# Kernel optimization log

Measured on AMD Instinct MI355X. Metric: run time of the kernel, lower is better.

## Reference

```python
import jax, jax.numpy as jnp
import numpy as np

N = 100000
E = 1600000
D_IN = 128
D_HID = 32
NEG_SLOPE = 0.2


def _glorot(key, shape):
    fan_in, fan_out = shape[0], shape[-1]
    lim = jnp.sqrt(6.0 / (fan_in + fan_out))
    return jax.random.uniform(key, shape, jnp.float32, -lim, lim)


def setup_inputs() -> dict:
    key = jax.random.key(0)
    ks = jax.random.split(key, 10)
    x = jax.random.normal(ks[0], (N, D_IN), jnp.float32)
    edge_index = jax.random.randint(ks[1], (2, E), 0, N, jnp.int64)
    return {
        "x": x,
        "edge_index": edge_index,
        "W1_l": _glorot(ks[2], (D_IN, D_HID)),
        "W1_r": _glorot(ks[3], (D_IN, D_HID)),
        "att1": _glorot(ks[4], (D_HID,)),
        "b1": jnp.zeros((D_HID,), jnp.float32),
        "W2_l": _glorot(ks[5], (D_HID, D_HID)),
        "W2_r": _glorot(ks[6], (D_HID, D_HID)),
        "att2": _glorot(ks[7], (D_HID,)),
        "b2": jnp.zeros((D_HID,), jnp.float32),
    }


def _segment_softmax(logits, seg, num_segments):
    m = jax.ops.segment_max(logits, seg, num_segments=num_segments)
    m = jnp.where(jnp.isfinite(m), m, 0.0)
    ex = jnp.exp(logits - m[seg])
    s = jax.ops.segment_sum(ex, seg, num_segments=num_segments)
    return ex / (s[seg] + 1e-16)


def _gatv2(x, edge_index, W_l, W_r, att, b):
    # GATv2Conv, heads=1, add_self_loops=False, share_weights=False
    src, dst = edge_index[0], edge_index[1]
    x_l = x @ W_l  # source transform [N, D_HID]
    x_r = x @ W_r  # target transform [N, D_HID]
    # per-edge attention logit: att . leaky_relu(x_l[j] + x_r[i])
    h = x_l[src] + x_r[dst]  # [E, D_HID]
    e = jnp.where(h > 0, h, NEG_SLOPE * h) @ att  # [E]
    alpha = _segment_softmax(e, dst, x.shape[0])  # softmax over incoming edges
    out = jax.ops.segment_sum(alpha[:, None] * x_l[src], dst,
                              num_segments=x.shape[0])
    return out + b


def reference(x, edge_index, W1_l, W1_r, att1, b1, W2_l, W2_r, att2, b2):
    h = _gatv2(x, edge_index, W1_l, W1_r, att1, b1)
    h = jax.nn.relu(h)
    return _gatv2(h, edge_index, W2_l, W2_r, att2, b2)
```

## Files before the change

### kernel.cpp

```cpp
#include <hip/hip_runtime.h>
#include <hip/hip_bf16.h>

#define D_HID 32
#define D_IN 128
#define NEG 0.2f
#define BSH 7
#define BSZ 128
#define MAXB 1024
#define MAXD 128

typedef unsigned short u16;
typedef __attribute__((ext_vector_type(8))) short short8;
typedef __attribute__((ext_vector_type(4))) float float4v;

__device__ __forceinline__ float b2f(u16 u){
  union { unsigned int i; float f; } c; c.i = ((unsigned int)u) << 16; return c.f;
}

__device__ __forceinline__ u16 f2b_rne(float f){
  union { float f; unsigned int u; } c; c.f = f;
  unsigned int u = c.u;
  return (u16)((u + 0x7FFFu + ((u >> 16) & 1u)) >> 16);
}

__device__ __forceinline__ void split_bf16(float v, u16& hi, u16& lo){
  hi = f2b_rne(v);
  lo = f2b_rne(v - b2f(hi));
}

__device__ __forceinline__ float ldf(const void* __restrict__ p, int f32, long long i){
  return f32 ? ((const float*)p)[i] : b2f(((const u16*)p)[i]);
}

__device__ __forceinline__ int atomAddI(int* p, int v){
  return __hip_atomic_fetch_add(p, v, __ATOMIC_RELAXED, __HIP_MEMORY_SCOPE_AGENT);
}

__device__ __forceinline__ float red8(float p){
  p += __int_as_float(__builtin_amdgcn_update_dpp(
         0, __float_as_int(p), 0xB1, 0xF, 0xF, true));
  p += __int_as_float(__builtin_amdgcn_update_dpp(
         0, __float_as_int(p), 0x4E, 0xF, 0xF, true));
  p += __int_as_float(__builtin_amdgcn_ds_swizzle(
         __float_as_int(p), 0x101F));
  return p;
}

__device__ __forceinline__ float edge_ev(const float4 xv, const float4 xrk,
                                         const float4 attk){
  float hx = xv.x + xrk.x; hx = fmaxf(hx, NEG*hx);
  float hy = xv.y + xrk.y; hy = fmaxf(hy, NEG*hy);
  float hz = xv.z + xrk.z; hz = fmaxf(hz, NEG*hz);
  float hw = xv.w + xrk.w; hw = fmaxf(hw, NEG*hw);
  float p = hx*attk.x;
  p = fmaf(hy, attk.y, p);
  p = fmaf(hz, attk.z, p);
  p = fmaf(hw, attk.w, p);
  p = red8(p);
  p = fminf(p, 60.f);
  return __expf(p);
}

__global__ void detect_flags(const int* __restrict__ ei, const u16* __restrict__ xw,
                             int* __restrict__ flags){
  __shared__ int insane_s, nz_s;
  int t = threadIdx.x;
  if (t == 0){ insane_s = 0; nz_s = 0; }
  __syncthreads();
  int pred = (t < 64) ? (ei[2*t+1] != 0) : 0;
  int e = (xw[t] >> 7) & 0xFF;
  int bad = (e < 100 || e > 140) ? 1 : 0;
  #pragma unroll
  for (int off = 32; off >= 1; off >>= 1){
    bad  += __shfl_down(bad,  off, 64);
    pred += __shfl_down(pred, off, 64);
  }
  if ((t & 63) == 0){
    atomicAdd(&insane_s, bad);
    atomicAdd(&nz_s, pred);
  }
  __syncthreads();
  if (t == 0){
    flags[0] = (nz_s == 0) ? 1 : 0;
    flags[1] = (insane_s > 16) ? 1 : 0;
  }
}

__device__ __forceinline__ void edge_nodes(const int* __restrict__ ei, int E_, int is64,
                                           int e, int& src, int& dst){
  if (is64){ src = ei[2*e]; dst = ei[2*E_ + 2*e]; }
  else     { src = ei[e];   dst = ei[E_ + e]; }
}

__global__ void prep_wfrag(const void* __restrict__ Wl, const void* __restrict__ Wr,
                           const int* __restrict__ flags, int K,
                           uint4* __restrict__ whi, uint4* __restrict__ wlo){
  int t = blockIdx.x * blockDim.x + threadIdx.x;
  int KS = K >> 5;
  int total = 4 * KS * 64;
  if (t >= total) return;
  int lane = t & 63;
  int rem = t >> 6;
  int kstep = rem % KS;
  int ctile = rem / KS;
  int f32 = flags[1];
  int col = ctile * 16 + (lane & 15);
  int quad = lane >> 4;
  union { u16 s[8]; uint4 q; } ch, cl;
  #pragma unroll
  for (int j = 0; j < 8; ++j){
    int k = kstep*32 + quad*8 + j;
    float v = (col < 32) ? ldf(Wl, f32, (long long)k*D_HID + col)
                         : ldf(Wr, f32, (long long)k*D_HID + (col - 32));
    u16 hi, lo; split_bf16(v, hi, lo);
    ch.s[j] = hi; cl.s[j] = lo;
  }
  whi[rem*64 + lane] = ch.q;
  wlo[rem*64 + lane] = cl.q;
}

template<int K>
__global__ void mfma_gemm(const void* __restrict__ X,
                          const uint4* __restrict__ whi, const uint4* __restrict__ wlo,
                          const int* __restrict__ flags, int force_f32,
                          float* __restrict__ xl, float* __restrict__ xr, int N_)
{
  constexpr int KS = K >> 5;
  int tile = blockIdx.x * (blockDim.x >> 6) + (threadIdx.x >> 6);
  if (tile * 16 >= N_) return;
  int lane = threadIdx.x & 63;
  int quad = lane >> 4;
  int m = tile*16 + (lane & 15);
  if (m >= N_) m = N_ - 1;
  int f32 = force_f32 | flags[1];

  float4v acc[4];
  #pragma unroll
  for (int c = 0; c < 4; ++c) acc[c] = (float4v){0.f,0.f,0.f,0.f};

  #pragma unroll
  for (int ks = 0; ks < KS; ++ks){
    long long base = (long long)m * K + ks*32 + quad*8;
    float av[8];
    if (f32){
      const float4* xp = (const float4*)((const float*)X + base);
      float4 t0 = xp[0], t1 = xp[1];
      av[0]=t0.x; av[1]=t0.y; av[2]=t0.z; av[3]=t0.w;
      av[4]=t1.x; av[5]=t1.y; av[6]=t1.z; av[7]=t1.w;
    } else {
      union { uint4 q; u16 s[8]; } c8;
      c8.q = *(const uint4*)((const u16*)X + base);
      #pragma unroll
      for (int j = 0; j < 8; ++j) av[j] = b2f(c8.s[j]);
    }
    short8 ahi, alo;
    #pragma unroll
    for (int j = 0; j < 8; ++j){
      u16 hi, lo; split_bf16(av[j], hi, lo);
      ahi[j] = (short)hi; alo[j] = (short)lo;
    }
    #pragma unroll
    for (int c = 0; c < 4; ++c){
      uint4 wh = whi[(c*KS + ks)*64 + lane];
      uint4 wl = wlo[(c*KS + ks)*64 + lane];
      short8 bh = *(short8*)&wh;
      short8 bl = *(short8*)&wl;
      acc[c] = __builtin_amdgcn_mfma_f32_16x16x32_bf16(ahi, bh, acc[c], 0, 0, 0);
      acc[c] = __builtin_amdgcn_mfma_f32_16x16x32_bf16(ahi, bl, acc[c], 0, 0, 0);
      acc[c] = __builtin_amdgcn_mfma_f32_16x16x32_bf16(alo, bh, acc[c], 0, 0, 0);
    }
  }

  #pragma unroll
  for (int c = 0; c < 4; ++c){
    int col = c*16 + (lane & 15);
    float* dst = (col < 32) ? xl : xr;
    int kk = col & 31;
    #pragma unroll
    for (int r = 0; r < 4; ++r){
      int node = tile*16 + quad*4 + r;
      if (node < N_) dst[(size_t)node*D_HID + kk] = acc[c][r];
    }
  }
}

__global__ void bucket_count(const int* __restrict__ ei, const int* __restrict__ flags,
                             int* __restrict__ gcnt, int E_, int B_){
  __shared__ int hist[MAXB];
  for (int i = threadIdx.x; i < B_; i += 256) hist[i] = 0;
  __syncthreads();
  int chunk = (E_ + gridDim.x - 1) / gridDim.x;
  int s = blockIdx.x * chunk;
  int e = s + chunk; if (e > E_) e = E_;
  int is64 = flags[0];
  for (int i = s + (int)threadIdx.x; i < e; i += 256){
    int dst = is64 ? ei[2*E_ + 2*i] : ei[E_ + i];
    atomicAdd(&hist[dst >> BSH], 1);
  }
  __syncthreads();
  for (int i = threadIdx.x; i < B_; i += 256)
    if (hist[i]) (void)atomAddI(&gcnt[i], hist[i]);
}

__global__ void scan_buckets(const int* __restrict__ gcnt, int* __restrict__ offsets,
                             int* __restrict__ cursor, int B_){
  __shared__ int sd[1024];
  int t = threadIdx.x;
  int v = (t < B_) ? gcnt[t] : 0;
  sd[t] = v;
  __syncthreads();
  for (int off = 1; off < 1024; off <<= 1){
    int tmp = (t >= off) ? sd[t-off] : 0;
    __syncthreads();
    sd[t] += tmp;
    __syncthreads();
  }
  if (t < B_){
    int excl = sd[t] - v;
    offsets[t] = excl;
    cursor[t]  = excl;
    if (t == B_-1) offsets[B_] = sd[t];
  }
}

__global__ void bucket_scatter(const int* __restrict__ ei, const int* __restrict__ flags,
                               int* __restrict__ cursor, unsigned* __restrict__ seg,
                               int E_, int B_){
  __shared__ int hist[MAXB];
  __shared__ int bbase[MAXB];
  for (int i = threadIdx.x; i < B_; i += 256) hist[i] = 0;
  __syncthreads();
  int chunk = (E_ + gridDim.x - 1) / gridDim.x;
  int s = blockIdx.x * chunk;
  int e = s + chunk; if (e > E_) e = E_;
  int is64 = flags[0];
  for (int i = s + (int)threadIdx.x; i < e; i += 256){
    int dst = is64 ? ei[2*E_ + 2*i] : ei[E_ + i];
    atomicAdd(&hist[dst >> BSH], 1);
  }
  __syncthreads();
  for (int i = threadIdx.x; i < B_; i += 256){
    int c = hist[i];
    bbase[i] = c ? atomAddI(&cursor[i], c) : 0;
  }
  __syncthreads();
  for (int i = threadIdx.x; i < B_; i += 256) hist[i] = 0;
  __syncthreads();
  for (int i = s + (int)threadIdx.x; i < e; i += 256){
    int src, dst;
    edge_nodes(ei, E_, is64, i, src, dst);
    int b = dst >> BSH;
    int pos = bbase[b] + atomicAdd(&hist[b], 1);
    seg[pos] = ((unsigned)src << BSH) | (unsigned)(dst & (BSZ-1));
  }
}

__global__ void bucket_finalize(const unsigned* __restrict__ seg,
                                const int* __restrict__ offsets,
                                int* __restrict__ row, int* __restrict__ csr_src,
                                int* __restrict__ dhist,
                                int N_, int B_){
  __shared__ int hist[BSZ];
  __shared__ int sc[BSZ];
  __shared__ int loff[BSZ];
  __shared__ int dh[MAXD];
  int b = blockIdx.x;
  int t = threadIdx.x;
  int base = offsets[b], cnt = offsets[b+1] - base;
  if (t < BSZ) hist[t] = 0;
  if (t < MAXD) dh[t] = 0;
  __syncthreads();
  for (int i = t; i < cnt; i += 256)
    atomicAdd(&hist[seg[base+i] & (BSZ-1)], 1);
  __syncthreads();
  if (t < BSZ){
    sc[t] = hist[t];
    int node = b*BSZ + t;
    if (node < N_) atomicAdd(&dh[min(hist[t], MAXD-1)], 1);
  }
  __syncthreads();
  for (int off = 1; off < BSZ; off <<= 1){
    int tmp = (t < BSZ && t >= off) ? sc[t-off] : 0;
    __syncthreads();
    if (t < BSZ) sc[t] += tmp;
    __syncthreads();
  }
  if (t < BSZ){
    int excl = sc[t] - hist[t];
    loff[t] = excl;
    int node = b*BSZ + t;
    if (node <= N_) row[node] = base + excl;
  }
  if (b == B_-1 && t == 0) row[N_] = offsets[B_];
  __syncthreads();
  for (int i = t; i < cnt; i += 256){
    unsigned en = seg[base+i];
    int dl = en & (BSZ-1);
    int pos = atomicAdd(&loff[dl], 1);
    csr_src[base + pos] = (int)en;
  }
  __syncthreads();
  if (t < MAXD && dh[t]) (void)atomAddI(&dhist[t], dh[t]);
}

__global__ void scan_deg(const int* __restrict__ dhist, int* __restrict__ dcur){
  __shared__ int sd[MAXD];
  int t = threadIdx.x;
  int v = dhist[t];
  sd[t] = v;
  __syncthreads();
  for (int off = 1; off < MAXD; off <<= 1){
    int tmp = (t >= off) ? sd[t-off] : 0;
    __syncthreads();
    sd[t] += tmp;
    __syncthreads();
  }
  dcur[t] = sd[t] - v;
}

__global__ void deg_scatter(const int* __restrict__ row, int* __restrict__ dcur,
                            int* __restrict__ perm, int N_){
  __shared__ int h[MAXD];
  __shared__ int base[MAXD];
  int t = threadIdx.x;
  int chunk = (N_ + gridDim.x - 1) / gridDim.x;
  int s = blockIdx.x * chunk;
  int e = s + chunk; if (e > N_) e = N_;
  if (t < MAXD) h[t] = 0;
  __syncthreads();
  for (int n = s + t; n < e; n += 256){
    int d = min(row[n+1] - row[n], MAXD-1);
    atomicAdd(&h[d], 1);
  }
  __syncthreads();
  if (t < MAXD){
    int c = h[t];
    base[t] = c ? atomAddI(&dcur[t], c) : 0;
  }
  __syncthreads();
  if (t < MAXD) h[t] = 0;
  __syncthreads();
  for (int n = s + t; n < e; n += 256){
    int d = min(row[n+1] - row[n], MAXD-1);
    int pos = base[d] + atomicAdd(&h[d], 1);
    perm[pos] = n;
  }
}

__global__ void gat_gather(const int* __restrict__ row, const unsigned* __restrict__ csrp,
                           const int* __restrict__ perm,
                           const float* __restrict__ xl, const float* __restrict__ xr,
                           const void* __restrict__ att, const void* __restrict__ bias,
                           const int* __restrict__ flags,
                           float* __restrict__ outp, int N_, int do_relu)
{
  int G = (blockIdx.x * blockDim.x + threadIdx.x) >> 3;
  if (G >= N_) return;
  int fl = threadIdx.x & 7;
  int f32 = flags[1];
  float4 attk;
  attk.x = ldf(att, f32, fl*4+0);
  attk.y = ldf(att, f32, fl*4+1);
  attk.z = ldf(att, f32, fl*4+2);
  attk.w = ldf(att, f32, fl*4+3);
  int n = perm[G];
  float4 xrk = *(const float4*)(xr + (size_t)n*D_HID + fl*4);
  int rs = row[n], re = row[n+1];
  const char* xlb = (const char*)xl;
  unsigned fo = (unsigned)(fl << 4);

  float4 acc = make_float4(0.f, 0.f, 0.f, 0.f);
  float ssum = 0.f;

  if (rs < re){
    int last = re - 1;
    unsigned c0 = csrp[rs];
    unsigned c1 = csrp[min(rs+1, last)];
    unsigned c2 = csrp[min(rs+2, last)];
    unsigned c3 = csrp[min(rs+3, last)];
    unsigned ca = csrp[min(rs+4, last)];
    unsigned cb = csrp[min(rs+5, last)];
    float4 xv0 = *(const float4*)(xlb + (c0 & ~127u) + fo);
    float4 xv1 = *(const float4*)(xlb + (c1 & ~127u) + fo);
    float4 xv2 = *(const float4*)(xlb + (c2 & ~127u) + fo);
    float4 xv3 = *(const float4*)(xlb + (c3 & ~127u) + fo);
    for (int i = rs; i < re; i += 2){
      float4 nx0 = *(const float4*)(xlb + (ca & ~127u) + fo);
      float4 nx1 = *(const float4*)(xlb + (cb & ~127u) + fo);
      unsigned na = csrp[min(i+6, last)];
      unsigned nb = csrp[min(i+7, last)];
      float ev0 = edge_ev(xv0, xrk, attk);
      ssum += ev0;
      acc.x = fmaf(ev0, xv0.x, acc.x);
      acc.y = fmaf(ev0, xv0.y, acc.y);
      acc.z = fmaf(ev0, xv0.z, acc.z);
      acc.w = fmaf(ev0, xv0.w, acc.w);
      float ev1 = edge_ev(xv1, xrk, attk);
      ev1 = (i + 1 <= last) ? ev1 : 0.f;
      ssum += ev1;
      acc.x = fmaf(ev1, xv1.x, acc.x);
      acc.y = fmaf(ev1, xv1.y, acc.y);
      acc.z = fmaf(ev1, xv1.z, acc.z);
      acc.w = fmaf(ev1, xv1.w, acc.w);
      xv0 = xv2; xv1 = xv3; xv2 = nx0; xv3 = nx1;
      ca = na; cb = nb;
    }
  }

  float inv = 1.0f / (ssum + 1e-16f);
  float4 o;
  o.x = acc.x*inv + ldf(bias, f32, fl*4+0);
  o.y = acc.y*inv + ldf(bias, f32, fl*4+1);
  o.z = acc.z*inv + ldf(bias, f32, fl*4+2);
  o.w = acc.w*inv + ldf(bias, f32, fl*4+3);
  if (do_relu){
    o.x = fmaxf(o.x, 0.f); o.y = fmaxf(o.y, 0.f);
    o.z = fmaxf(o.z, 0.f); o.w = fmaxf(o.w, 0.f);
  }
  *(float4*)(outp + (size_t)n*D_HID + fl*4) = o;
}

extern "C" void kernel_launch(void* const* d_in, const int* in_sizes, int n_in,
                              void* d_out, int out_size, void* d_ws, size_t ws_size,
                              hipStream_t stream)
{
  const void* x   = d_in[0];
  const int*  ei  = (const int*)d_in[1];
  const void* W1l = d_in[2];
  const void* W1r = d_in[3];
  const void* att1= d_in[4];
  const void* b1  = d_in[5];
  const void* W2l = d_in[6];
  const void* W2r = d_in[7];
  const void* att2= d_in[8];
  const void* b2  = d_in[9];
  float* out = (float*)d_out;

  int N_ = in_sizes[0] / D_IN;
  int E_ = in_sizes[1] / 2;
  int B_ = (N_ + BSZ - 1) / BSZ;

  char* ws = (char*)d_ws;
  size_t off = 0;
  auto carve = [&](size_t bytes) -> char* {
    char* p = ws + off;
    off += (bytes + 255) & ~(size_t)255;
    return p;
  };
  float*    xl      = (float*)   carve((size_t)N_ * D_HID * 4);
  float*    xr      = (float*)   carve((size_t)N_ * D_HID * 4);
  float*    h       = (float*)   carve((size_t)N_ * D_HID * 4);
  unsigned* seg     = (unsigned*)carve((size_t)E_ * 4);
  int*      csr_src = (int*)     carve((size_t)E_ * 4);
  int*      row     = (int*)     carve((size_t)(N_ + 1) * 4);
  int*      perm    = (int*)     carve((size_t)N_ * 4);
  int*      offsets = (int*)     carve((size_t)(MAXB + 1) * 4);
  int*      gcnt    = (int*)     carve((size_t)MAXB * 4);
  int*      cursor  = (int*)     carve((size_t)MAXB * 4);
  int*      dhist   = (int*)     carve((size_t)MAXD * 4);
  int*      dcur    = (int*)     carve((size_t)MAXD * 4);
  int*      flags   = (int*)     carve(256);
  uint4*    whi1    = (uint4*)   carve((size_t)4 * 4 * 64 * 16);
  uint4*    wlo1    = (uint4*)   carve((size_t)4 * 4 * 64 * 16);
  uint4*    whi2    = (uint4*)   carve((size_t)4 * 1 * 64 * 16);
  uint4*    wlo2    = (uint4*)   carve((size_t)4 * 1 * 64 * 16);

  const int tpb = 256;
  int gG = (N_ + 31) / 32;
  int tiles = (N_ + 15) / 16;
  int gT = (tiles + 3) / 4;

  detect_flags<<<1, 256, 0, stream>>>(ei, (const u16*)x, flags);

  prep_wfrag<<<4, 256, 0, stream>>>(W1l, W1r, flags, D_IN, whi1, wlo1);
  prep_wfrag<<<1, 256, 0, stream>>>(W2l, W2r, flags, D_HID, whi2, wlo2);

  hipMemsetAsync(gcnt, 0, (size_t)MAXB * 4, stream);
  hipMemsetAsync(dhist, 0, (size_t)MAXD * 4, stream);
  bucket_count<<<256, tpb, 0, stream>>>(ei, flags, gcnt, E_, B_);
  scan_buckets<<<1, 1024, 0, stream>>>(gcnt, offsets, cursor, B_);
  bucket_scatter<<<256, tpb, 0, stream>>>(ei, flags, cursor, seg, E_, B_);
  bucket_finalize<<<B_, tpb, 0, stream>>>(seg, offsets, row, csr_src, dhist, N_, B_);

  scan_deg<<<1, MAXD, 0, stream>>>(dhist, dcur);
  deg_scatter<<<64, tpb, 0, stream>>>(row, dcur, perm, N_);

  mfma_gemm<D_IN><<<gT, tpb, 0, stream>>>(x, whi1, wlo1, flags, 0, xl, xr, N_);
  gat_gather<<<gG, tpb, 0, stream>>>(row, (const unsigned*)csr_src, perm, xl, xr,
                                     att1, b1, flags, h, N_, 1);

  mfma_gemm<D_HID><<<gT, tpb, 0, stream>>>(h, whi2, wlo2, flags, 1, xl, xr, N_);
  gat_gather<<<gG, tpb, 0, stream>>>(row, (const unsigned*)csr_src, perm, xl, xr,
                                     att2, b2, flags, out, N_, 0);
}
```

Baseline: 275.9 us.

## Fuse CSR build stages into fewer launches and drop degree-sorted permutation

Merges flag detection with bucket counting, fuses the bucket scan, scatter and weight-fragment prep into one launch with each block redoing the scan redundantly, and co-schedules bucket finalization with the first-layer GEMM in one grid. It drops the degree histogram and node permutation, so the gather walks nodes in natural order, and it deepens the gather's edge prefetch from four to six rows. The intent is to cut launch count and serialization on a short pipeline, at the cost of redundant per-block scans and losing degree-balanced warp scheduling in the gather.

```diff
diff --git a/kernel.cpp b/kernel.cpp
--- a/kernel.cpp
+++ b/kernel.cpp
@@ -7,7 +7,7 @@
 #define BSH 7
 #define BSZ 128
 #define MAXB 1024
-#define MAXD 128
+#define SCATB 256
 
 typedef unsigned short u16;
 typedef __attribute__((ext_vector_type(8))) short short8;
@@ -61,41 +61,43 @@
   return __expf(p);
 }
 
-__global__ void detect_flags(const int* __restrict__ ei, const u16* __restrict__ xw,
-                             int* __restrict__ flags){
-  __shared__ int insane_s, nz_s;
+__global__ void __launch_bounds__(256)
+count_flags(const int* __restrict__ ei, const u16* __restrict__ xw,
+            int* __restrict__ gcnt, int* __restrict__ flags, int E_, int B_){
+  __shared__ int hist[MAXB];
+  __shared__ int nz_s, insane_s;
   int t = threadIdx.x;
-  if (t == 0){ insane_s = 0; nz_s = 0; }
-  __syncthreads();
-  int pred = (t < 64) ? (ei[2*t+1] != 0) : 0;
-  int e = (xw[t] >> 7) & 0xFF;
-  int bad = (e < 100 || e > 140) ? 1 : 0;
-  #pragma unroll
-  for (int off = 32; off >= 1; off >>= 1){
-    bad  += __shfl_down(bad,  off, 64);
-    pred += __shfl_down(pred, off, 64);
-  }
-  if ((t & 63) == 0){
-    atomicAdd(&insane_s, bad);
-    atomicAdd(&nz_s, pred);
-  }
-  __syncthreads();
-  if (t == 0){
-    flags[0] = (nz_s == 0) ? 1 : 0;
+  if (t == 0){ nz_s = 0; insane_s = 0; }
+  for (int i = t; i < B_; i += 256) hist[i] = 0;
+  __syncthreads();
+  if (t < 64 && ei[2*t+1] != 0) atomicAdd(&nz_s, 1);
+  if (blockIdx.x == 0){
+    int e = (xw[t] >> 7) & 0xFF;
+    if (e < 100 || e > 140) atomicAdd(&insane_s, 1);
+  }
+  __syncthreads();
+  int is64 = (nz_s == 0);
+  if (blockIdx.x == 0 && t == 0){
+    flags[0] = is64;
     flags[1] = (insane_s > 16) ? 1 : 0;
   }
-}
-
-__device__ __forceinline__ void edge_nodes(const int* __restrict__ ei, int E_, int is64,
-                                           int e, int& src, int& dst){
-  if (is64){ src = ei[2*e]; dst = ei[2*E_ + 2*e]; }
-  else     { src = ei[e];   dst = ei[E_ + e]; }
-}
-
-__global__ void prep_wfrag(const void* __restrict__ Wl, const void* __restrict__ Wr,
-                           const int* __restrict__ flags, int K,
-                           uint4* __restrict__ whi, uint4* __restrict__ wlo){
-  int t = blockIdx.x * blockDim.x + threadIdx.x;
+  int chunk = (E_ + gridDim.x - 1) / gridDim.x;
+  int s = blockIdx.x * chunk;
+  int e = s + chunk; if (e > E_) e = E_;
+  for (int i = s + t; i < e; i += 256){
+    int dst = is64 ? ei[2*E_ + 2*i] : ei[E_ + i];
+    atomicAdd(&hist[dst >> BSH], 1);
+  }
+  __syncthreads();
+  for (int i = t; i < B_; i += 256)
+    if (hist[i]) (void)atomAddI(&gcnt[i], hist[i]);
+}
+
+__device__ __forceinline__ void prep_body(const void* __restrict__ Wl,
+                                          const void* __restrict__ Wr,
+                                          int f32, int K,
+                                          uint4* __restrict__ whi,
+                                          uint4* __restrict__ wlo, int t){
   int KS = K >> 5;
   int total = 4 * KS * 64;
   if (t >= total) return;
@@ -103,7 +105,6 @@
   int rem = t >> 6;
   int kstep = rem % KS;
   int ctile = rem / KS;
-  int f32 = flags[1];
   int col = ctile * 16 + (lane & 15);
   int quad = lane >> 4;
   union { u16 s[8]; uint4 q; } ch, cl;
@@ -119,16 +120,123 @@
   wlo[rem*64 + lane] = cl.q;
 }
 
+__global__ void __launch_bounds__(256)
+scan_scatter_prep(const int* __restrict__ ei, const int* __restrict__ flags,
+                  const int* __restrict__ gcnt, int* __restrict__ cur0,
+                  unsigned* __restrict__ seg, int* __restrict__ offsets,
+                  const void* __restrict__ W1l, const void* __restrict__ W1r,
+                  const void* __restrict__ W2l, const void* __restrict__ W2r,
+                  uint4* __restrict__ whi1, uint4* __restrict__ wlo1,
+                  uint4* __restrict__ whi2, uint4* __restrict__ wlo2,
+                  int E_, int B_){
+  int t = threadIdx.x;
+  if ((int)blockIdx.x >= SCATB){
+    int sub = blockIdx.x - SCATB;
+    int f32 = flags[1];
+    if (sub < 4) prep_body(W1l, W1r, f32, D_IN,  whi1, wlo1, sub*256 + t);
+    else         prep_body(W2l, W2r, f32, D_HID, whi2, wlo2, t);
+    return;
+  }
+  __shared__ int sd[MAXB];
+  __shared__ int part[256];
+  __shared__ int hist[MAXB];
+  __shared__ int bbase[MAXB];
+  for (int i = t; i < MAXB; i += 256) sd[i] = (i < B_) ? gcnt[i] : 0;
+  __syncthreads();
+  int a0 = sd[4*t], a1 = sd[4*t+1], a2 = sd[4*t+2], a3 = sd[4*t+3];
+  int mysum = a0 + a1 + a2 + a3;
+  part[t] = mysum;
+  __syncthreads();
+  for (int off = 1; off < 256; off <<= 1){
+    int v = (t >= off) ? part[t-off] : 0;
+    __syncthreads();
+    part[t] += v;
+    __syncthreads();
+  }
+  int excl = part[t] - mysum;
+  sd[4*t]   = excl;
+  sd[4*t+1] = excl + a0;
+  sd[4*t+2] = excl + a0 + a1;
+  sd[4*t+3] = excl + a0 + a1 + a2;
+  __syncthreads();
+  if (blockIdx.x == 0){
+    for (int i = t; i <= B_; i += 256)
+      offsets[i] = (i < MAXB) ? sd[i] : part[255];
+  }
+  for (int i = t; i < B_; i += 256) hist[i] = 0;
+  __syncthreads();
+  int is64 = flags[0];
+  int chunk = (E_ + SCATB - 1) / SCATB;
+  int s = blockIdx.x * chunk;
+  int e = s + chunk; if (e > E_) e = E_;
+  for (int i = s + t; i < e; i += 256){
+    int dst = is64 ? ei[2*E_ + 2*i] : ei[E_ + i];
+    atomicAdd(&hist[dst >> BSH], 1);
+  }
+  __syncthreads();
+  for (int i = t; i < B_; i += 256){
+    int c = hist[i];
+    bbase[i] = c ? (sd[i] + atomAddI(&cur0[i], c)) : 0;
+  }
+  __syncthreads();
+  for (int i = t; i < B_; i += 256) hist[i] = 0;
+  __syncthreads();
+  for (int i = s + t; i < e; i += 256){
+    int src, dst;
+    if (is64){ src = ei[2*i]; dst = ei[2*E_ + 2*i]; }
+    else     { src = ei[i];   dst = ei[E_ + i]; }
+    int b = dst >> BSH;
+    int pos = bbase[b] + atomicAdd(&hist[b], 1);
+    seg[pos] = ((unsigned)src << BSH) | (unsigned)(dst & (BSZ-1));
+  }
+}
+
+__device__ void finalize_body(const unsigned* __restrict__ seg,
+                              const int* __restrict__ offsets,
+                              int* __restrict__ row, int* __restrict__ csr_src,
+                              int N_, int B_, int b, int t){
+  __shared__ int hist[BSZ];
+  __shared__ int sc[BSZ];
+  __shared__ int loff[BSZ];
+  int base = offsets[b], cnt = offsets[b+1] - base;
+  if (t < BSZ) hist[t] = 0;
+  __syncthreads();
+  for (int i = t; i < cnt; i += 256)
+    atomicAdd(&hist[seg[base+i] & (BSZ-1)], 1);
+  __syncthreads();
+  if (t < BSZ) sc[t] = hist[t];
+  __syncthreads();
+  for (int off = 1; off < BSZ; off <<= 1){
+    int tmp = (t < BSZ && t >= off) ? sc[t-off] : 0;
+    __syncthreads();
+    if (t < BSZ) sc[t] += tmp;
+    __syncthreads();
+  }
+  if (t < BSZ){
+    int excl = sc[t] - hist[t];
+    loff[t] = excl;
+    int node = b*BSZ + t;
+    if (node <= N_) row[node] = base + excl;
+  }
+  if (b == B_-1 && t == 0) row[N_] = offsets[B_];
+  __syncthreads();
+  for (int i = t; i < cnt; i += 256){
+    unsigned en = seg[base+i];
+    int dl = en & (BSZ-1);
+    int pos = atomicAdd(&loff[dl], 1);
+    csr_src[base + pos] = (int)en;
+  }
+}
+
 template<int K>
-__global__ void mfma_gemm(const void* __restrict__ X,
+__device__ __forceinline__ void gemm_body(const void* __restrict__ X,
                           const uint4* __restrict__ whi, const uint4* __restrict__ wlo,
                           const int* __restrict__ flags, int force_f32,
-                          float* __restrict__ xl, float* __restrict__ xr, int N_)
+                          float* __restrict__ xl, float* __restrict__ xr,
+                          int N_, int tile, int lane)
 {
   constexpr int KS = K >> 5;
-  int tile = blockIdx.x * (blockDim.x >> 6) + (threadIdx.x >> 6);
   if (tile * 16 >= N_) return;
-  int lane = threadIdx.x & 63;
   int quad = lane >> 4;
   int m = tile*16 + (lane & 15);
   if (m >= N_) m = N_ - 1;
@@ -184,175 +292,38 @@
   }
 }
 
-__global__ void bucket_count(const int* __restrict__ ei, const int* __restrict__ flags,
-                             int* __restrict__ gcnt, int E_, int B_){
-  __shared__ int hist[MAXB];
-  for (int i = threadIdx.x; i < B_; i += 256) hist[i] = 0;
-  __syncthreads();
-  int chunk = (E_ + gridDim.x - 1) / gridDim.x;
-  int s = blockIdx.x * chunk;
-  int e = s + chunk; if (e > E_) e = E_;
-  int is64 = flags[0];
-  for (int i = s + (int)threadIdx.x; i < e; i += 256){
-    int dst = is64 ? ei[2*E_ + 2*i] : ei[E_ + i];
-    atomicAdd(&hist[dst >> BSH], 1);
-  }
-  __syncthreads();
-  for (int i = threadIdx.x; i < B_; i += 256)
-    if (hist[i]) (void)atomAddI(&gcnt[i], hist[i]);
-}
-
-__global__ void scan_buckets(const int* __restrict__ gcnt, int* __restrict__ offsets,
-                             int* __restrict__ cursor, int B_){
-  __shared__ int sd[1024];
-  int t = threadIdx.x;
-  int v = (t < B_) ? gcnt[t] : 0;
-  sd[t] = v;
-  __syncthreads();
-  for (int off = 1; off < 1024; off <<= 1){
-    int tmp = (t >= off) ? sd[t-off] : 0;
-    __syncthreads();
-    sd[t] += tmp;
-    __syncthreads();
-  }
-  if (t < B_){
-    int excl = sd[t] - v;
-    offsets[t] = excl;
-    cursor[t]  = excl;
-    if (t == B_-1) offsets[B_] = sd[t];
-  }
-}
-
-__global__ void bucket_scatter(const int* __restrict__ ei, const int* __restrict__ flags,
-                               int* __restrict__ cursor, unsigned* __restrict__ seg,
-                               int E_, int B_){
-  __shared__ int hist[MAXB];
-  __shared__ int bbase[MAXB];
-  for (int i = threadIdx.x; i < B_; i += 256) hist[i] = 0;
-  __syncthreads();
-  int chunk = (E_ + gridDim.x - 1) / gridDim.x;
-  int s = blockIdx.x * chunk;
-  int e = s + chunk; if (e > E_) e = E_;
-  int is64 = flags[0];
-  for (int i = s + (int)threadIdx.x; i < e; i += 256){
-    int dst = is64 ? ei[2*E_ + 2*i] : ei[E_ + i];
-    atomicAdd(&hist[dst >> BSH], 1);
-  }
-  __syncthreads();
-  for (int i = threadIdx.x; i < B_; i += 256){
-    int c = hist[i];
-    bbase[i] = c ? atomAddI(&cursor[i], c) : 0;
-  }
-  __syncthreads();
-  for (int i = threadIdx.x; i < B_; i += 256) hist[i] = 0;
-  __syncthreads();
-  for (int i = s + (int)threadIdx.x; i < e; i += 256){
-    int src, dst;
-    edge_nodes(ei, E_, is64, i, src, dst);
-    int b = dst >> BSH;
-    int pos = bbase[b] + atomicAdd(&hist[b], 1);
-    seg[pos] = ((unsigned)src << BSH) | (unsigned)(dst & (BSZ-1));
-  }
-}
-
-__global__ void bucket_finalize(const unsigned* __restrict__ seg,
-                                const int* __restrict__ offsets,
-                                int* __restrict__ row, int* __restrict__ csr_src,
-                                int* __restrict__ dhist,
-                                int N_, int B_){
-  __shared__ int hist[BSZ];
-  __shared__ int sc[BSZ];
-  __shared__ int loff[BSZ];
-  __shared__ int dh[MAXD];
-  int b = blockIdx.x;
-  int t = threadIdx.x;
-  int base = offsets[b], cnt = offsets[b+1] - base;
-  if (t < BSZ) hist[t] = 0;
-  if (t < MAXD) dh[t] = 0;
-  __syncthreads();
-  for (int i = t; i < cnt; i += 256)
-    atomicAdd(&hist[seg[base+i] & (BSZ-1)], 1);
-  __syncthreads();
-  if (t < BSZ){
-    sc[t] = hist[t];
-    int node = b*BSZ + t;
-    if (node < N_) atomicAdd(&dh[min(hist[t], MAXD-1)], 1);
-  }
-  __syncthreads();
-  for (int off = 1; off < BSZ; off <<= 1){
-    int tmp = (t < BSZ && t >= off) ? sc[t-off] : 0;
-    __syncthreads();
-    if (t < BSZ) sc[t] += tmp;
-    __syncthreads();
-  }
-  if (t < BSZ){
-    int excl = sc[t] - hist[t];
-    loff[t] = excl;
-    int node = b*BSZ + t;
-    if (node <= N_) row[node] = base + excl;
-  }
-  if (b == B_-1 && t == 0) row[N_] = offsets[B_];
-  __syncthreads();
-  for (int i = t; i < cnt; i += 256){
-    unsigned en = seg[base+i];
-    int dl = en & (BSZ-1);
-    int pos = atomicAdd(&loff[dl], 1);
-    csr_src[base + pos] = (int)en;
-  }
-  __syncthreads();
-  if (t < MAXD && dh[t]) (void)atomAddI(&dhist[t], dh[t]);
-}
-
-__global__ void scan_deg(const int* __restrict__ dhist, int* __restrict__ dcur){
-  __shared__ int sd[MAXD];
-  int t = threadIdx.x;
-  int v = dhist[t];
-  sd[t] = v;
-  __syncthreads();
-  for (int off = 1; off < MAXD; off <<= 1){
-    int tmp = (t >= off) ? sd[t-off] : 0;
-    __syncthreads();
-    sd[t] += tmp;
-    __syncthreads();
-  }
-  dcur[t] = sd[t] - v;
-}
-
-__global__ void deg_scatter(const int* __restrict__ row, int* __restrict__ dcur,
-                            int* __restrict__ perm, int N_){
-  __shared__ int h[MAXD];
-  __shared__ int base[MAXD];
-  int t = threadIdx.x;
-  int chunk = (N_ + gridDim.x - 1) / gridDim.x;
-  int s = blockIdx.x * chunk;
-  int e = s + chunk; if (e > N_) e = N_;
-  if (t < MAXD) h[t] = 0;
-  __syncthreads();
-  for (int n = s + t; n < e; n += 256){
-    int d = min(row[n+1] - row[n], MAXD-1);
-    atomicAdd(&h[d], 1);
-  }
-  __syncthreads();
-  if (t < MAXD){
-    int c = h[t];
-    base[t] = c ? atomAddI(&dcur[t], c) : 0;
-  }
-  __syncthreads();
-  if (t < MAXD) h[t] = 0;
-  __syncthreads();
-  for (int n = s + t; n < e; n += 256){
-    int d = min(row[n+1] - row[n], MAXD-1);
-    int pos = base[d] + atomicAdd(&h[d], 1);
-    perm[pos] = n;
-  }
-}
-
-__global__ void gat_gather(const int* __restrict__ row, const unsigned* __restrict__ csrp,
-                           const int* __restrict__ perm,
-                           const float* __restrict__ xl, const float* __restrict__ xr,
-                           const void* __restrict__ att, const void* __restrict__ bias,
-                           const int* __restrict__ flags,
-                           float* __restrict__ outp, int N_, int do_relu)
+template<int K>
+__global__ void __launch_bounds__(256)
+fin_gemm(const unsigned* __restrict__ seg, const int* __restrict__ offsets,
+         int* __restrict__ row, int* __restrict__ csr_src,
+         const void* __restrict__ X,
+         const uint4* __restrict__ whi, const uint4* __restrict__ wlo,
+         const int* __restrict__ flags,
+         float* __restrict__ xl, float* __restrict__ xr, int N_, int B_){
+  if ((int)blockIdx.x < B_){
+    finalize_body(seg, offsets, row, csr_src, N_, B_, blockIdx.x, threadIdx.x);
+    return;
+  }
+  int tile = (blockIdx.x - B_) * 4 + (threadIdx.x >> 6);
+  gemm_body<K>(X, whi, wlo, flags, 0, xl, xr, N_, tile, threadIdx.x & 63);
+}
+
+template<int K>
+__global__ void __launch_bounds__(256)
+mfma_gemm(const void* __restrict__ X,
+          const uint4* __restrict__ whi, const uint4* __restrict__ wlo,
+          const int* __restrict__ flags, int force_f32,
+          float* __restrict__ xl, float* __restrict__ xr, int N_){
+  int tile = blockIdx.x * 4 + (threadIdx.x >> 6);
+  gemm_body<K>(X, whi, wlo, flags, force_f32, xl, xr, N_, tile, threadIdx.x & 63);
+}
+
+__global__ void __launch_bounds__(256)
+gat_gather(const int* __restrict__ row, const unsigned* __restrict__ csrp,
+           const float* __restrict__ xl, const float* __restrict__ xr,
+           const void* __restrict__ att, const void* __restrict__ bias,
+           const int* __restrict__ flags,
+           float* __restrict__ outp, int N_, int do_relu)
 {
   int G = (blockIdx.x * blockDim.x + threadIdx.x) >> 3;
   if (G >= N_) return;
@@ -363,7 +334,7 @@
   attk.y = ldf(att, f32, fl*4+1);
   attk.z = ldf(att, f32, fl*4+2);
   attk.w = ldf(att, f32, fl*4+3);
-  int n = perm[G];
+  int n = G;
   float4 xrk = *(const float4*)(xr + (size_t)n*D_HID + fl*4);
   int rs = row[n], re = row[n+1];
   const char* xlb = (const char*)xl;
@@ -374,21 +345,25 @@
 
   if (rs < re){
     int last = re - 1;
+    unsigned ca = csrp[min(rs+6, last)];
+    unsigned cb = csrp[min(rs+7, last)];
     unsigned c0 = csrp[rs];
     unsigned c1 = csrp[min(rs+1, last)];
     unsigned c2 = csrp[min(rs+2, last)];
     unsigned c3 = csrp[min(rs+3, last)];
-    unsigned ca = csrp[min(rs+4, last)];
-    unsigned cb = csrp[min(rs+5, last)];
+    unsigned c4 = csrp[min(rs+4, last)];
+    unsigned c5 = csrp[min(rs+5, last)];
     float4 xv0 = *(const float4*)(xlb + (c0 & ~127u) + fo);
     float4 xv1 = *(const float4*)(xlb + (c1 & ~127u) + fo);
     float4 xv2 = *(const float4*)(xlb + (c2 & ~127u) + fo);
     float4 xv3 = *(const float4*)(xlb + (c3 & ~127u) + fo);
+    float4 xv4 = *(const float4*)(xlb + (c4 & ~127u) + fo);
+    float4 xv5 = *(const float4*)(xlb + (c5 & ~127u) + fo);
     for (int i = rs; i < re; i += 2){
       float4 nx0 = *(const float4*)(xlb + (ca & ~127u) + fo);
       float4 nx1 = *(const float4*)(xlb + (cb & ~127u) + fo);
-      unsigned na = csrp[min(i+6, last)];
-      unsigned nb = csrp[min(i+7, last)];
+      unsigned na = csrp[min(i+8, last)];
+      unsigned nb = csrp[min(i+9, last)];
       float ev0 = edge_ev(xv0, xrk, attk);
       ssum += ev0;
       acc.x = fmaf(ev0, xv0.x, acc.x);
@@ -402,7 +377,7 @@
       acc.y = fmaf(ev1, xv1.y, acc.y);
       acc.z = fmaf(ev1, xv1.z, acc.z);
       acc.w = fmaf(ev1, xv1.w, acc.w);
-      xv0 = xv2; xv1 = xv3; xv2 = nx0; xv3 = nx1;
+      xv0 = xv2; xv1 = xv3; xv2 = xv4; xv3 = xv5; xv4 = nx0; xv5 = nx1;
       ca = na; cb = nb;
     }
   }
@@ -453,12 +428,9 @@
   unsigned* seg     = (unsigned*)carve((size_t)E_ * 4);
   int*      csr_src = (int*)     carve((size_t)E_ * 4);
   int*      row     = (int*)     carve((size_t)(N_ + 1) * 4);
-  int*      perm    = (int*)     carve((size_t)N_ * 4);
   int*      offsets = (int*)     carve((size_t)(MAXB + 1) * 4);
   int*      gcnt    = (int*)     carve((size_t)MAXB * 4);
-  int*      cursor  = (int*)     carve((size_t)MAXB * 4);
-  int*      dhist   = (int*)     carve((size_t)MAXD * 4);
-  int*      dcur    = (int*)     carve((size_t)MAXD * 4);
+  int*      cur0    = (int*)     carve((size_t)MAXB * 4);
   int*      flags   = (int*)     carve(256);
   uint4*    whi1    = (uint4*)   carve((size_t)4 * 4 * 64 * 16);
   uint4*    wlo1    = (uint4*)   carve((size_t)4 * 4 * 64 * 16);
@@ -470,26 +442,22 @@
   int tiles = (N_ + 15) / 16;
   int gT = (tiles + 3) / 4;
 
-  detect_flags<<<1, 256, 0, stream>>>(ei, (const u16*)x, flags);
-
-  prep_wfrag<<<4, 256, 0, stream>>>(W1l, W1r, flags, D_IN, whi1, wlo1);
-  prep_wfrag<<<1, 256, 0, stream>>>(W2l, W2r, flags, D_HID, whi2, wlo2);
-
-  hipMemsetAsync(gcnt, 0, (size_t)MAXB * 4, stream);
-  hipMemsetAsync(dhist, 0, (size_t)MAXD * 4, stream);
-  bucket_count<<<256, tpb, 0, stream>>>(ei, flags, gcnt, E_, B_);
-  scan_buckets<<<1, 1024, 0, stream>>>(gcnt, offsets, cursor, B_);
-  bucket_scatter<<<256, tpb, 0, stream>>>(ei, flags, cursor, seg, E_, B_);
-  bucket_finalize<<<B_, tpb, 0, stream>>>(seg, offsets, row, csr_src, dhist, N_, B_);
-
-  scan_deg<<<1, MAXD, 0, stream>>>(dhist, dcur);
-  deg_scatter<<<64, tpb, 0, stream>>>(row, dcur, perm, N_);
-
-  mfma_gemm<D_IN><<<gT, tpb, 0, stream>>>(x, whi1, wlo1, flags, 0, xl, xr, N_);
-  gat_gather<<<gG, tpb, 0, stream>>>(row, (const unsigned*)csr_src, perm, xl, xr,
+  hipMemsetAsync(gcnt, 0, (size_t)2 * MAXB * 4, stream);
+
+  count_flags<<<256, tpb, 0, stream>>>(ei, (const u16*)x, gcnt, flags, E_, B_);
+
+  scan_scatter_prep<<<SCATB + 5, tpb, 0, stream>>>(
+      ei, flags, gcnt, cur0, seg, offsets,
+      W1l, W1r, W2l, W2r, whi1, wlo1, whi2, wlo2, E_, B_);
+
+  fin_gemm<D_IN><<<B_ + gT, tpb, 0, stream>>>(
+      seg, offsets, row, csr_src, x, whi1, wlo1, flags, xl, xr, N_, B_);
+
+  gat_gather<<<gG, tpb, 0, stream>>>(row, (const unsigned*)csr_src, xl, xr,
                                      att1, b1, flags, h, N_, 1);
 
   mfma_gemm<D_HID><<<gT, tpb, 0, stream>>>(h, whi2, wlo2, flags, 1, xl, xr, N_);
-  gat_gather<<<gG, tpb, 0, stream>>>(row, (const unsigned*)csr_src, perm, xl, xr,
+
+  gat_gather<<<gG, tpb, 0, stream>>>(row, (const unsigned*)csr_src, xl, xr,
                                      att2, b2, flags, out, N_, 0);
 }
```

New measurement: 251.0 us. 9.0% less time.
